# Kernel tuning notes

Measured on AMD Instinct MI355X. Metric: run time of the kernel, lower is better.

Reference implementation:

```python
import jax, jax.numpy as jnp
import numpy as np

N_NODES = 100000


def gcn_conv(x, edge_index, W, b, n_nodes):
    """PyG GCNConv: add self-loops, symmetric deg norm, linear, scatter-add, bias."""
    self_loops = jnp.arange(n_nodes, dtype=edge_index.dtype)
    src = jnp.concatenate([edge_index[0], self_loops])  # [E+N]
    dst = jnp.concatenate([edge_index[1], self_loops])  # [E+N]
    xw = x @ W  # [N, out]
    deg = jax.ops.segment_sum(jnp.ones_like(dst, dtype=xw.dtype), dst, num_segments=n_nodes)
    deg_inv_sqrt = jnp.where(deg > 0, jax.lax.rsqrt(deg), 0.0)
    norm = deg_inv_sqrt[src] * deg_inv_sqrt[dst]  # [E+N]
    msg = xw[src] * norm[:, None]                 # [E+N, out]
    out = jax.ops.segment_sum(msg, dst, num_segments=n_nodes)
    return out + b


def setup_inputs() -> dict:
    key = jax.random.key(0)
    ks = jax.random.split(key, 8)
    n, e, d_in, h = N_NODES, 3200000, 128, 16
    x = jax.random.normal(ks[0], (n, d_in), dtype=jnp.float32)
    edge_index = jax.random.randint(ks[1], (2, e), 0, n, dtype=jnp.int64)
    W1 = jax.random.normal(ks[2], (d_in, h), dtype=jnp.float32) / np.sqrt(d_in)
    b1 = jnp.zeros((h,), dtype=jnp.float32)
    W2 = jax.random.normal(ks[3], (h, h), dtype=jnp.float32) / np.sqrt(h)
    b2 = jnp.zeros((h,), dtype=jnp.float32)
    W_lin = jax.random.normal(ks[4], (h, 1), dtype=jnp.float32) / np.sqrt(h)
    b_lin = jnp.zeros((1,), dtype=jnp.float32)
    return {"x": x, "edge_index": edge_index, "W1": W1, "b1": b1,
            "W2": W2, "b2": b2, "W_lin": W_lin, "b_lin": b_lin}


def reference(x, edge_index, W1, b1, W2, b2, W_lin, b_lin):
    n = x.shape[0]
    h = gcn_conv(x, edge_index, W1, b1, n)
    h = jax.nn.relu(h)
    # dropout is identity in eval mode (training=False)
    h = gcn_conv(h, edge_index, W2, b2, n)
    h = jax.nn.relu(h)
    out = h @ W_lin + b_lin  # [N, 1]
    return out.squeeze(-1)   # [N]
```

## Files before the change

### kernel.cpp

```cpp
#include <hip/hip_runtime.h>

#define DIN 128
#define HDIM 16
#define NB 256
#define CAP 13312
#define CAPC 14848
#define BIN_EPT 16

__device__ __forceinline__ float4 f4add(float4 a, float4 b) {
    return make_float4(a.x + b.x, a.y + b.y, a.z + b.z, a.w + b.w);
}

__device__ __forceinline__ int load_idx(const void* ei, long long i, int is64) {
    return is64 ? (int)((const long long*)ei)[i] : ((const int*)ei)[i];
}

__global__ __launch_bounds__(256) void k_main(const void* __restrict__ ei, long long E,
                                              int bdiv, int* __restrict__ bcur,
                                              unsigned int* __restrict__ recs,
                                              const float* __restrict__ x,
                                              const float* __restrict__ W1,
                                              float* __restrict__ y1,
                                              int n, int nbin) {
    __shared__ int cnt[NB];
    __shared__ int base[NB];
    __shared__ float Ws[DIN * HDIM];
    int tid = threadIdx.x;
    if ((int)blockIdx.x < nbin) {
        unsigned probe = ((const unsigned*)ei)[1 + 2 * (tid & 63)];
        int is64 = (__ballot(probe != 0) == 0ull) ? 1 : 0;
        if (tid < NB) cnt[tid] = 0;
        __syncthreads();
        long long e0 = (long long)blockIdx.x * (256 * BIN_EPT);
        int s[BIN_EPT], d[BIN_EPT], b[BIN_EPT];
#pragma unroll
        for (int i = 0; i < BIN_EPT; i++) {
            long long e = e0 + (long long)i * 256 + tid;
            if (e < E) {
                s[i] = load_idx(ei, e, is64);
                d[i] = load_idx(ei, E + e, is64);
                b[i] = (int)((unsigned)d[i] / (unsigned)bdiv);
                atomicAdd(&cnt[b[i]], 1);
            } else {
                b[i] = -1;
            }
        }
        __syncthreads();
        if (tid < NB) {
            base[tid] = atomicAdd(&bcur[tid], cnt[tid]);
            cnt[tid] = 0;
        }
        __syncthreads();
#pragma unroll
        for (int i = 0; i < BIN_EPT; i++) {
            if (b[i] >= 0) {
                int off = atomicAdd(&cnt[b[i]], 1);
                int pos = base[b[i]] + off;
                if (pos < CAP) {
                    unsigned int dloc = (unsigned)(d[i] - b[i] * bdiv);
                    recs[(size_t)b[i] * CAP + pos] = (dloc << 18) | (unsigned)s[i];
                }
            }
        }
    } else {
        for (int i = tid; i < DIN * HDIM; i += 256) Ws[i] = W1[i];
        __syncthreads();
        int node = ((int)blockIdx.x - nbin) * 256 + tid;
        if (node > n) return;
        float4* yr = (float4*)(y1 + (size_t)node * HDIM);
        if (node == n) {
            float4 z = make_float4(0.f, 0.f, 0.f, 0.f);
#pragma unroll
            for (int q = 0; q < 4; q++) yr[q] = z;
            return;
        }
        float acc[HDIM];
#pragma unroll
        for (int f = 0; f < HDIM; f++) acc[f] = 0.f;
        const float4* xr = (const float4*)(x + (size_t)node * DIN);
#pragma unroll 8
        for (int k4 = 0; k4 < DIN / 4; k4++) {
            float4 xv = xr[k4];
            int k = k4 * 4;
#pragma unroll
            for (int f = 0; f < HDIM; f++) {
                acc[f] += xv.x * Ws[(k + 0) * HDIM + f];
                acc[f] += xv.y * Ws[(k + 1) * HDIM + f];
                acc[f] += xv.z * Ws[(k + 2) * HDIM + f];
                acc[f] += xv.w * Ws[(k + 3) * HDIM + f];
            }
        }
#pragma unroll
        for (int q = 0; q < 4; q++)
            yr[q] = make_float4(acc[q * 4 + 0], acc[q * 4 + 1],
                                acc[q * 4 + 2], acc[q * 4 + 3]);
    }
}

__global__ __launch_bounds__(512) void k_prep(const unsigned int* __restrict__ recs,
                                              const int* __restrict__ bcur,
                                              float* __restrict__ dis,
                                              unsigned int* __restrict__ meta,
                                              int* __restrict__ col,
                                              float* __restrict__ y1,
                                              int bdiv, int n) {
    __shared__ int cnt_sh[512];
    __shared__ int sc[512];
    __shared__ unsigned short buf[CAPC];
    int tid = threadIdx.x;
    int b = blockIdx.x;
    int lo = b * bdiv; if (lo > n) lo = n;
    int hi = lo + bdiv; if (hi > n) hi = n;
    int nd = hi - lo;
    cnt_sh[tid] = 0;
    __syncthreads();
    int m = bcur[b]; if (m > CAP) m = CAP;
    const unsigned int* r = recs + (size_t)b * CAP;
    for (int i = tid; i < m; i += 512)
        atomicAdd(&cnt_sh[r[i] >> 18], 1);
    __syncthreads();
    int v  = (tid < nd) ? cnt_sh[tid] : 0;
    int pv = (v + 3) & ~3;
    sc[tid] = pv;
    __syncthreads();
    for (int off = 1; off < 512; off <<= 1) {
        int t = (tid >= off) ? sc[tid - off] : 0;
        __syncthreads();
        sc[tid] += t;
        __syncthreads();
    }
    int ptot = sc[511];
    if (tid < nd) {
        int excl = sc[tid] - pv;
        dis[lo + tid] = rsqrtf((float)v + 1.0f);
        meta[lo + tid] = ((unsigned)(b * CAPC + excl) << 10) | (unsigned)v;
        cnt_sh[tid] = excl;
    }
    for (int i = tid; i < ptot; i += 512) buf[i] = 0xFFFFu;
    __syncthreads();
    for (int i = tid; i < m; i += 512) {
        int pos = atomicAdd(&cnt_sh[r[i] >> 18], 1);
        buf[pos] = (unsigned short)i;
    }
    __syncthreads();
    for (int i = tid; i < ptot; i += 512) {
        unsigned short bi = buf[i];
        col[b * CAPC + i] = (bi == 0xFFFFu) ? n : (int)(r[bi] & 0x3FFFFu);
    }
    int q = tid & 3, slot = tid >> 2;
    float4* yv = (float4*)y1;
    for (int j = slot; j < nd; j += 128) {
        int node = lo + j;
        float dv = dis[node];
        float4 t = yv[(size_t)node * 4 + q];
        yv[(size_t)node * 4 + q] =
            make_float4(t.x * dv, t.y * dv, t.z * dv, t.w * dv);
    }
}

__global__ __launch_bounds__(256) void k_gather1(const unsigned int* __restrict__ meta,
                                                 const int* __restrict__ col,
                                                 const float* __restrict__ y1,
                                                 const float* __restrict__ dis,
                                                 const float* __restrict__ b1,
                                                 const float* __restrict__ W2,
                                                 float* __restrict__ y2, int n) {
    __shared__ float4 Ws4[HDIM][4];
    if (threadIdx.x < HDIM * 4)
        ((float4*)Ws4)[threadIdx.x] = ((const float4*)W2)[threadIdx.x];
    __syncthreads();
    if (blockIdx.x == 0 && threadIdx.x < 4)
        ((float4*)y2)[(size_t)n * 4 + threadIdx.x] = make_float4(0.f, 0.f, 0.f, 0.f);
    int ln = threadIdx.x >> 2;
    int q  = threadIdx.x & 3;
    int node = blockIdx.x * 64 + ln;
    if (node >= n) return;
    unsigned mt = meta[node];
    int start = (int)(mt >> 10);
    int endp  = start + (((int)(mt & 1023u) + 3) & ~3);
    const float4* yv = (const float4*)y1;
    float4 a0 = make_float4(0.f, 0.f, 0.f, 0.f), a1 = a0, a2 = a0, a3 = a0;
    int e = start;
    for (; e + 16 <= endp; e += 16) {
        int4 c4 = *(const int4*)(col + e + 4 * q);
        int s[16];
#pragma unroll
        for (int j = 0; j < 4; j++) {
            s[4 * j + 0] = __shfl(c4.x, j, 4);
            s[4 * j + 1] = __shfl(c4.y, j, 4);
            s[4 * j + 2] = __shfl(c4.z, j, 4);
            s[4 * j + 3] = __shfl(c4.w, j, 4);
        }
        float4 v[16];
#pragma unroll
        for (int k = 0; k < 16; k++) v[k] = yv[(size_t)s[k] * 4 + q];
#pragma unroll
        for (int k = 0; k < 16; k += 4) {
            a0 = f4add(a0, v[k + 0]); a1 = f4add(a1, v[k + 1]);
            a2 = f4add(a2, v[k + 2]); a3 = f4add(a3, v[k + 3]);
        }
    }
    for (; e < endp; e += 4) {
        int4 c4 = *(const int4*)(col + e);
        float4 v0 = yv[(size_t)c4.x * 4 + q];
        float4 v1 = yv[(size_t)c4.y * 4 + q];
        float4 v2 = yv[(size_t)c4.z * 4 + q];
        float4 v3 = yv[(size_t)c4.w * 4 + q];
        a0 = f4add(a0, v0); a1 = f4add(a1, v1);
        a2 = f4add(a2, v2); a3 = f4add(a3, v3);
    }
    float4 acc = f4add(f4add(a0, a1), f4add(a2, a3));
    acc = f4add(acc, yv[(size_t)node * 4 + q]);
    float dv = dis[node];
    float4 bb = ((const float4*)b1)[q];
    float4 h;
    h.x = fmaxf(dv * acc.x + bb.x, 0.f);
    h.y = fmaxf(dv * acc.y + bb.y, 0.f);
    h.z = fmaxf(dv * acc.z + bb.z, 0.f);
    h.w = fmaxf(dv * acc.w + bb.w, 0.f);
    float4 o = make_float4(0.f, 0.f, 0.f, 0.f);
#pragma unroll
    for (int k = 0; k < 4; k++) {
        float4 hk;
        hk.x = __shfl(h.x, k, 4); hk.y = __shfl(h.y, k, 4);
        hk.z = __shfl(h.z, k, 4); hk.w = __shfl(h.w, k, 4);
        float hv[4] = {hk.x, hk.y, hk.z, hk.w};
#pragma unroll
        for (int c = 0; c < 4; c++) {
            float4 w = Ws4[k * 4 + c][q];
            o.x += hv[c] * w.x; o.y += hv[c] * w.y;
            o.z += hv[c] * w.z; o.w += hv[c] * w.w;
        }
    }
    ((float4*)y2)[(size_t)node * 4 + q] =
        make_float4(o.x * dv, o.y * dv, o.z * dv, o.w * dv);
}

__global__ __launch_bounds__(256) void k_gather2(const unsigned int* __restrict__ meta,
                                                 const int* __restrict__ col,
                                                 const float* __restrict__ y2,
                                                 const float* __restrict__ dis,
                                                 const float* __restrict__ b2,
                                                 const float* __restrict__ Wlin,
                                                 const float* __restrict__ blin,
                                                 float* __restrict__ out, int n) {
    int ln = threadIdx.x >> 2;
    int q  = threadIdx.x & 3;
    int node = blockIdx.x * 64 + ln;
    if (node >= n) return;
    unsigned mt = meta[node];
    int start = (int)(mt >> 10);
    int endp  = start + (((int)(mt & 1023u) + 3) & ~3);
    const float4* yv = (const float4*)y2;
    float4 a0 = make_float4(0.f, 0.f, 0.f, 0.f), a1 = a0, a2 = a0, a3 = a0;
    int e = start;
    for (; e + 16 <= endp; e += 16) {
        int4 c4 = *(const int4*)(col + e + 4 * q);
        int s[16];
#pragma unroll
        for (int j = 0; j < 4; j++) {
            s[4 * j + 0] = __shfl(c4.x, j, 4);
            s[4 * j + 1] = __shfl(c4.y, j, 4);
            s[4 * j + 2] = __shfl(c4.z, j, 4);
            s[4 * j + 3] = __shfl(c4.w, j, 4);
        }
        float4 v[16];
#pragma unroll
        for (int k = 0; k < 16; k++) v[k] = yv[(size_t)s[k] * 4 + q];
#pragma unroll
        for (int k = 0; k < 16; k += 4) {
            a0 = f4add(a0, v[k + 0]); a1 = f4add(a1, v[k + 1]);
            a2 = f4add(a2, v[k + 2]); a3 = f4add(a3, v[k + 3]);
        }
    }
    for (; e < endp; e += 4) {
        int4 c4 = *(const int4*)(col + e);
        float4 v0 = yv[(size_t)c4.x * 4 + q];
        float4 v1 = yv[(size_t)c4.y * 4 + q];
        float4 v2 = yv[(size_t)c4.z * 4 + q];
        float4 v3 = yv[(size_t)c4.w * 4 + q];
        a0 = f4add(a0, v0); a1 = f4add(a1, v1);
        a2 = f4add(a2, v2); a3 = f4add(a3, v3);
    }
    float4 acc = f4add(f4add(a0, a1), f4add(a2, a3));
    acc = f4add(acc, yv[(size_t)node * 4 + q]);
    float dv = dis[node];
    float4 bb = ((const float4*)b2)[q];
    float4 wl = ((const float4*)Wlin)[q];
    float v = 0.f;
    v += fmaxf(dv * acc.x + bb.x, 0.f) * wl.x;
    v += fmaxf(dv * acc.y + bb.y, 0.f) * wl.y;
    v += fmaxf(dv * acc.z + bb.z, 0.f) * wl.z;
    v += fmaxf(dv * acc.w + bb.w, 0.f) * wl.w;
    v += __shfl_xor(v, 1, 4);
    v += __shfl_xor(v, 2, 4);
    if (q == 0) out[node] = v + blin[0];
}

extern "C" void kernel_launch(void* const* d_in, const int* in_sizes, int n_in,
                              void* d_out, int out_size, void* d_ws, size_t ws_size,
                              hipStream_t stream) {
    const float* x    = (const float*)d_in[0];
    const void*  ei   = d_in[1];
    const float* W1   = (const float*)d_in[2];
    const float* b1   = (const float*)d_in[3];
    const float* W2   = (const float*)d_in[4];
    const float* b2   = (const float*)d_in[5];
    const float* Wlin = (const float*)d_in[6];
    const float* blin = (const float*)d_in[7];
    float* out = (float*)d_out;

    const int n = in_sizes[0] / DIN;
    const long long E = in_sizes[1] / 2;
    const int bdiv = (n + NB - 1) / NB;

    char* ws = (char*)d_ws;
    size_t off = 0;
    auto alloc = [&](size_t bytes) { char* p = ws + off; off += (bytes + 255) & ~(size_t)255; return p; };
    int*   bcur   = (int*)alloc(NB * 4);
    float* dis    = (float*)alloc((size_t)n * 4);
    unsigned int* meta = (unsigned int*)alloc((size_t)n * 4);
    float* y1     = (float*)alloc((size_t)(n + 1) * HDIM * 4);
    size_t region_elems = (size_t)NB * CAP;
    if (region_elems < (size_t)(n + 1) * HDIM) region_elems = (size_t)(n + 1) * HDIM;
    char*  region = alloc(region_elems * 4);
    unsigned int* recs = (unsigned int*)region;
    float* y2     = (float*)region;
    int*   col    = (int*)alloc((size_t)NB * CAPC * 4);

    const int nb_xw  = (n + 1 + 255) / 256;
    const int nb_bin = (int)((E + 256 * BIN_EPT - 1) / (256 * BIN_EPT));
    const int nb_g   = (n + 63) / 64;

    hipMemsetAsync(bcur, 0, NB * sizeof(int), stream);
    k_main<<<nb_bin + nb_xw, 256, 0, stream>>>(ei, E, bdiv, bcur, recs, x, W1, y1, n, nb_bin);
    k_prep<<<NB, 512, 0, stream>>>(recs, bcur, dis, meta, col, y1, bdiv, n);
    k_gather1<<<nb_g, 256, 0, stream>>>(meta, col, y1, dis, b1, W2, y2, n);
    k_gather2<<<nb_g, 256, 0, stream>>>(meta, col, y2, dis, b2, Wlin, blin, out, n);
}
```

Measured before the change: 228.1 us.

## Stage binned edge records in LDS and write coalesced; double bucket count

The binning kernel now sorts each block's 4096 edges by bucket in shared memory, using a block-wide prefix scan over bucket counts, before writing them out. Each bucket's records then go to global memory as contiguous runs instead of scattered single writes. The bucket count doubles to 512 with smaller per-bucket capacities, which changes the granularity of the downstream prep and gather kernels. The cost is a larger shared-memory footprint per block and an extra scan with several barriers.

Result: slower. 246.8 us (+8.2%).

```diff
diff --git a/kernel.cpp b/kernel.cpp
--- a/kernel.cpp
+++ b/kernel.cpp
@@ -2,10 +2,10 @@
 
 #define DIN 128
 #define HDIM 16
-#define NB 256
-#define CAP 13312
-#define CAPC 14848
-#define BIN_EPT 16
+#define NB 512
+#define CAP 7168
+#define CAPC 7952
+#define BIN_SMEM 32768
 
 __device__ __forceinline__ float4 f4add(float4 a, float4 b) {
     return make_float4(a.x + b.x, a.y + b.y, a.z + b.z, a.w + b.w);
@@ -22,47 +22,74 @@
                                               const float* __restrict__ W1,
                                               float* __restrict__ y1,
                                               int n, int nbin) {
-    __shared__ int cnt[NB];
-    __shared__ int base[NB];
-    __shared__ float Ws[DIN * HDIM];
+    __shared__ __align__(16) char smem[BIN_SMEM];
     int tid = threadIdx.x;
     if ((int)blockIdx.x < nbin) {
+        int* cnt    = (int*)smem;
+        int* base   = cnt + NB;
+        int* lstart = base + NB;
+        int* sc     = lstart + NB;
+        unsigned* rbuf = (unsigned*)(sc + 256);
+        unsigned short* bkt = (unsigned short*)(rbuf + 4096);
         unsigned probe = ((const unsigned*)ei)[1 + 2 * (tid & 63)];
         int is64 = (__ballot(probe != 0) == 0ull) ? 1 : 0;
-        if (tid < NB) cnt[tid] = 0;
-        __syncthreads();
-        long long e0 = (long long)blockIdx.x * (256 * BIN_EPT);
-        int s[BIN_EPT], d[BIN_EPT], b[BIN_EPT];
-#pragma unroll
-        for (int i = 0; i < BIN_EPT; i++) {
-            long long e = e0 + (long long)i * 256 + tid;
+        cnt[tid] = 0; cnt[tid + 256] = 0;
+        __syncthreads();
+        long long e0 = (long long)blockIdx.x * 4096;
+        int s[16], d[16], bb[16];
+#pragma unroll
+        for (int i = 0; i < 16; i++) {
+            long long e = e0 + i * 256 + tid;
             if (e < E) {
                 s[i] = load_idx(ei, e, is64);
                 d[i] = load_idx(ei, E + e, is64);
-                b[i] = (int)((unsigned)d[i] / (unsigned)bdiv);
-                atomicAdd(&cnt[b[i]], 1);
-            } else {
-                b[i] = -1;
+            } else s[i] = -1;
+        }
+#pragma unroll
+        for (int i = 0; i < 16; i++) {
+            if (s[i] >= 0) {
+                bb[i] = (int)((unsigned)d[i] / (unsigned)bdiv);
+                atomicAdd(&cnt[bb[i]], 1);
+            } else bb[i] = -1;
+        }
+        __syncthreads();
+        int c0 = cnt[2 * tid], c1 = cnt[2 * tid + 1];
+        int pair = c0 + c1;
+        sc[tid] = pair;
+        __syncthreads();
+        for (int off = 1; off < 256; off <<= 1) {
+            int t = (tid >= off) ? sc[tid - off] : 0;
+            __syncthreads();
+            sc[tid] += t;
+            __syncthreads();
+        }
+        int ep = sc[tid] - pair;
+        lstart[2 * tid] = ep;
+        lstart[2 * tid + 1] = ep + c0;
+        base[2 * tid]     = atomicAdd(&bcur[2 * tid], c0);
+        base[2 * tid + 1] = atomicAdd(&bcur[2 * tid + 1], c1);
+        cnt[2 * tid] = 0; cnt[2 * tid + 1] = 0;
+        __syncthreads();
+        int ptot = sc[255];
+#pragma unroll
+        for (int i = 0; i < 16; i++) {
+            if (bb[i] >= 0) {
+                int off = atomicAdd(&cnt[bb[i]], 1);
+                int pos = lstart[bb[i]] + off;
+                unsigned dloc = (unsigned)(d[i] - bb[i] * bdiv);
+                rbuf[pos] = (dloc << 18) | (unsigned)s[i];
+                bkt[pos] = (unsigned short)bb[i];
             }
         }
         __syncthreads();
-        if (tid < NB) {
-            base[tid] = atomicAdd(&bcur[tid], cnt[tid]);
-            cnt[tid] = 0;
-        }
-        __syncthreads();
-#pragma unroll
-        for (int i = 0; i < BIN_EPT; i++) {
-            if (b[i] >= 0) {
-                int off = atomicAdd(&cnt[b[i]], 1);
-                int pos = base[b[i]] + off;
-                if (pos < CAP) {
-                    unsigned int dloc = (unsigned)(d[i] - b[i] * bdiv);
-                    recs[(size_t)b[i] * CAP + pos] = (dloc << 18) | (unsigned)s[i];
-                }
-            }
+        for (int i = tid; i < ptot; i += 256) {
+            int b = bkt[i];
+            int gpos = base[b] + (i - lstart[b]);
+            if (gpos < CAP)
+                recs[(size_t)b * CAP + gpos] = rbuf[i];
         }
     } else {
+        float* Ws = (float*)smem;
         for (int i = tid; i < DIN * HDIM; i += 256) Ws[i] = W1[i];
         __syncthreads();
         int node = ((int)blockIdx.x - nbin) * 256 + tid;
@@ -329,7 +356,7 @@
     int*   col    = (int*)alloc((size_t)NB * CAPC * 4);
 
     const int nb_xw  = (n + 1 + 255) / 256;
-    const int nb_bin = (int)((E + 256 * BIN_EPT - 1) / (256 * BIN_EPT));
+    const int nb_bin = (int)((E + 4095) / 4096);
     const int nb_g   = (n + 63) / 64;
 
     hipMemsetAsync(bcur, 0, NB * sizeof(int), stream);
```
